# Optimization experiments

Hardware: AMD Instinct MI355X
Metric: run time of the kernel (lower is better)

## Reference

```python
import jax, jax.numpy as jnp
import numpy as np

B, N, NV = 2, 4096, 32768
HID = 128
XD, YD, ZD = 128, 128, 16  # dense occupancy grid dims (original derives from coord maxima)


def setup_inputs() -> dict:
    key = jax.random.key(0)
    ks = jax.random.split(key, 12)
    position = jax.random.normal(ks[0], (B, N, 3), jnp.float32) * 20.0
    scale = jax.random.uniform(ks[1], (B, N, 3), jnp.float32)
    rotation = jax.random.normal(ks[2], (B, N, 4), jnp.float32)
    opacity = jax.random.uniform(ks[3], (B, N, 1), jnp.float32)
    # sparse voxel coords: [batch_idx, x, y, z]
    b_idx = jax.random.randint(ks[4], (NV, 1), 0, B)
    xs = jax.random.randint(ks[5], (NV, 1), 0, XD)
    ys = jax.random.randint(ks[6], (NV, 1), 0, YD)
    zs = jax.random.randint(ks[7], (NV, 1), 0, ZD)
    voxel_coords = jnp.concatenate([b_idx, xs, ys, zs], axis=1).astype(jnp.int32)
    # MLP params: Linear(11,128) -> ReLU -> Linear(128,128)
    W1 = jax.random.normal(ks[8], (11, HID), jnp.float32) * (1.0 / np.sqrt(11))
    b1 = jnp.zeros((HID,), jnp.float32)
    W2 = jax.random.normal(ks[9], (HID, HID), jnp.float32) * (1.0 / np.sqrt(HID))
    b2 = jnp.zeros((HID,), jnp.float32)
    return {"position": position, "scale": scale, "rotation": rotation,
            "opacity": opacity, "W1": W1, "b1": b1, "W2": W2, "b2": b2,
            "voxel_coords": voxel_coords}


def reference(position, scale, rotation, opacity, W1, b1, W2, b2, voxel_coords):
    # concat gaussian attributes -> (B, N, 11)
    x = jnp.concatenate([position, scale, rotation, opacity], axis=-1)
    x = jnp.maximum(x @ W1 + b1, 0.0) @ W2 + b2  # (B, N, HID)

    # anchor grid: linspace(-50,50, N^(1/3))^3 -> (N, 3)
    n_side = int(round(N ** (1.0 / 3.0)))
    anchor_pos = jnp.linspace(-50.0, 50.0, n_side)
    grid = jnp.stack(jnp.meshgrid(anchor_pos, anchor_pos, anchor_pos, indexing="ij"), axis=-1)
    anchor_grid = grid.reshape(-1, 3)  # (N, 3)

    batch_ids = voxel_coords[:, 0]
    xyz = voxel_coords[:, 1:].astype(jnp.float32)  # (NV, 3)

    # Euclidean cdist (NV, N) via ||a||^2 + ||b||^2 - 2ab
    d2 = (jnp.sum(xyz * xyz, axis=1, keepdims=True)
          + jnp.sum(anchor_grid * anchor_grid, axis=1)[None, :]
          - 2.0 * (xyz @ anchor_grid.T))
    dist = jnp.sqrt(jnp.maximum(d2, 0.0))
    weight = jax.nn.softmax(-dist, axis=-1)  # (NV, N)

    fused = jnp.einsum("vn,bnd->bvd", weight, x)  # (B, NV, HID)

    # scatter into dense 5D occupancy grid (vectorized over all batches)
    occ = jnp.zeros((B, HID, XD, YD, ZD), jnp.float32)
    vals = fused[batch_ids, jnp.arange(NV)]  # (NV, HID) per-voxel feature from its own batch
    occ = occ.at[batch_ids, :, voxel_coords[:, 1], voxel_coords[:, 2], voxel_coords[:, 3]].set(vals)
    return occ
```

## Files before the change

kernel.cpp:

```cpp
#include <hip/hip_runtime.h>
#include <hip/hip_bf16.h>

#define B_    2
#define N_    4096
#define NV_   32768
#define HID_  128
#define XD_   128
#define YD_   128
#define ZD_   16
#define PLANE (XD_*YD_*ZD_)
#define LOCS  (B_*PLANE)
#define STEP  (100.0f/15.0f)
#define KS    4
#define VBL   160
#define L2E   1.4426950408889634f

typedef __attribute__((ext_vector_type(8)))  short short8;
typedef __attribute__((ext_vector_type(16))) float f32x16;

__device__ __forceinline__ float anchor_s(int i) {
    return fmaf((float)i, STEP * L2E, -50.0f * L2E);
}
__device__ __forceinline__ float fexp2(float x) {
    float r; asm("v_exp_f32 %0, %1" : "=v"(r) : "v"(x)); return r;
}
__device__ __forceinline__ unsigned short f2bf(float x) {
    unsigned u = __float_as_uint(x);
    return (unsigned short)((u + 0x7fffu + ((u >> 16) & 1u)) >> 16);
}
__device__ __forceinline__ void gload16(const void* g, void* l) {
    __builtin_amdgcn_global_load_lds(
        (const __attribute__((address_space(1))) unsigned int*)g,
        (__attribute__((address_space(3))) unsigned int*)l, 16, 0, 0);
}

__global__ __launch_bounds__(256) void mlp_kernel(
    const float* __restrict__ pos, const float* __restrict__ scl,
    const float* __restrict__ rot, const float* __restrict__ opa,
    const float* __restrict__ W1,  const float* __restrict__ b1,
    const float* __restrict__ W2,  const float* __restrict__ b2,
    unsigned short* __restrict__ xwT)
{
    int rg = threadIdx.x >> 7;
    int j  = threadIdx.x & 127;
    int r  = blockIdx.x * 2 + rg;
    __shared__ float sin_[2][11];
    __shared__ float h[2][HID_];
    if (j < 11) {
        float val;
        if (j < 3)       val = pos[r*3 + j];
        else if (j < 6)  val = scl[r*3 + (j-3)];
        else if (j < 10) val = rot[r*4 + (j-6)];
        else             val = opa[r];
        sin_[rg][j] = val;
    }
    __syncthreads();
    float a = b1[j];
    #pragma unroll
    for (int i = 0; i < 11; ++i) a = fmaf(sin_[rg][i], W1[i*HID_ + j], a);
    h[rg][j] = fmaxf(a, 0.0f);
    __syncthreads();
    float o = b2[j];
    for (int k = 0; k < HID_; ++k) o = fmaf(h[rg][k], W2[k*HID_ + j], o);
    int b = r >> 12, n = r & 4095;
    xwT[((size_t)(b*HID_ + j))*N_ + n] = f2bf(o);
}

__global__ __launch_bounds__(256) void scatter_kernel(
    const int* __restrict__ vc, int* __restrict__ map,
    int* __restrict__ cnt, int* __restrict__ vlist)
{
    int v = blockIdx.x * 256 + threadIdx.x;
    int4 c = ((const int4*)vc)[v];
    int loc = ((c.x*XD_ + c.y)*YD_ + c.z)*ZD_ + c.w;
    atomicMax(&map[loc], v);
    int lane = threadIdx.x & 63;
    unsigned long long m1 = __ballot(c.x != 0);
    unsigned long long mymask = c.x ? m1 : ~m1;
    int leader = (int)__ffsll(mymask) - 1;
    int total  = __popcll(mymask);
    int rank   = __popcll(mymask & ((1ull << lane) - 1ull));
    int base = 0;
    if (lane == leader) base = atomicAdd(&cnt[c.x], total);
    base = __shfl(base, leader);
    vlist[c.x*NV_ + base + rank] = v;
}

__global__ __launch_bounds__(256) void ml_kernel(
    const int* __restrict__ vc, float2* __restrict__ ml)
{
    int gid = blockIdx.x * 256 + threadIdx.x;
    int v = gid >> 3, sub = gid & 7;
    int4 c = ((const int4*)vc)[v];
    float vx = (float)c.y * L2E, vy = (float)c.z * L2E, vz = (float)c.w * L2E;
    float dz2_[16];
    #pragma unroll 16
    for (int iz = 0; iz < 16; ++iz) { float t = vz - anchor_s(iz); dz2_[iz] = t*t; }

    float m = 1e30f, l = 0.0f;
    #pragma unroll
    for (int i = 0; i < 2; ++i) {
        float dx = vx - anchor_s(sub*2 + i);
        float dx2 = dx*dx;
        for (int iy = 0; iy < 16; ++iy) {
            float dy = vy - anchor_s(iy);
            float bxy = fmaf(dy, dy, dx2);
            #pragma unroll 16
            for (int iz = 0; iz < 16; ++iz) {
                float d = sqrtf(bxy + dz2_[iz]);
                float dm = d - m;
                float e = fexp2(-fabsf(dm));
                bool nm = dm < 0.0f;
                l = nm ? fmaf(l, e, 1.0f) : (l + e);
                m = nm ? d : m;
            }
        }
    }
    #pragma unroll
    for (int off = 1; off < 8; off <<= 1) {
        float m2 = __shfl_xor(m, off);
        float l2 = __shfl_xor(l, off);
        float mn = fminf(m, m2);
        l = l * fexp2(mn - m) + l2 * fexp2(mn - m2);
        m = mn;
    }
    if (sub == 0) ml[v] = make_float2(m, 1.0f / l);
}

__global__ __launch_bounds__(256) void fuse_kernel(
    const unsigned short* __restrict__ xwT, const float2* __restrict__ ml,
    const int* __restrict__ vc,   const int* __restrict__ vlist,
    const int* __restrict__ cnt,  float* __restrict__ fused_p)
{
    int bid  = blockIdx.x;
    int ks_  = bid & (KS-1);
    int rest = bid >> 2;
    int seg  = (rest >= VBL) ? 1 : 0;
    int bi   = rest - seg*VBL;
    int count = cnt[seg];
    int vbase = bi * 128;
    if (vbase >= count) return;
    int nv = min(128, count - vbase);
    int k0 = ks_ * (N_/KS);

    __shared__ __align__(16) unsigned char sXT[16384];
    __shared__ int svid[128];

    int tid = threadIdx.x;
    int w  = tid >> 6, l = tid & 63;
    int h  = l >> 5;
    int cl = l & 31;

    if (tid < 128) svid[tid] = (tid < nv) ? vlist[seg*NV_ + vbase + tid] : -1;

    int vloc = w*32 + cl;
    float pml = -1e30f, pvx = 0.f, pvy = 0.f;
    float dz2_[16];
    #pragma unroll 16
    for (int iz = 0; iz < 16; ++iz) dz2_[iz] = 0.f;
    if (vloc < nv) {
        int vid = vlist[seg*NV_ + vbase + vloc];
        int4 c = ((const int4*)vc)[vid];
        pvx = (float)c.y * L2E; pvy = (float)c.z * L2E;
        float pvz = (float)c.w * L2E;
        pml = ml[vid].x;
        #pragma unroll 16
        for (int iz = 0; iz < 16; ++iz) { float t = pvz - anchor_s(iz); dz2_[iz] = t*t; }
    }

    int d0s  = w*32 + (l >> 3);
    int blkX = (l & 7) ^ ((l >> 3) & 7);
    const unsigned short* sb = xwT + (size_t)(seg*128 + d0s)*N_ + blkX*8 + k0;
    char* ldsb = (char*)sXT + (size_t)(w*4)*1024;

    f32x16 acc[4];
    #pragma unroll
    for (int i = 0; i < 4; ++i) acc[i] = (f32x16)(0.f);

    for (int t = 0; t < (N_/KS)/64; ++t) {
        __syncthreads();
        #pragma unroll
        for (int i = 0; i < 4; ++i)
            gload16(sb + (size_t)i*8*N_ + t*64, ldsb + i*1024);

        unsigned pk_[4][4];
        int nb = k0 + t*64;
        #pragma unroll
        for (int kss = 0; kss < 4; ++kss) {
            int kg = nb + kss*16;
            float ax = anchor_s(kg >> 8);
            float ay = anchor_s((kg >> 4) & 15);
            float dx = pvx - ax, dy = pvy - ay;
            float bxy = fmaf(dx, dx, dy*dy);
            #pragma unroll
            for (int jj = 0; jj < 4; ++jj) {
                float dA = sqrtf(bxy + dz2_[h*8 + 2*jj]);
                float dB = sqrtf(bxy + dz2_[h*8 + 2*jj + 1]);
                float p0 = fexp2(pml - dA);
                float p1 = fexp2(pml - dB);
                asm("v_cvt_pk_bf16_f32 %0, %1, %2" : "=v"(pk_[kss][jj]) : "v"(p0), "v"(p1));
            }
        }
        __syncthreads();

        #pragma unroll
        for (int kss = 0; kss < 4; ++kss) {
            union { uint4 q; short8 s; } u8;
            u8.q = make_uint4(pk_[kss][0], pk_[kss][1], pk_[kss][2], pk_[kss][3]);
            short8 af = u8.s;
            #pragma unroll
            for (int df = 0; df < 4; ++df) {
                int row = df*32 + cl;
                int blk = (kss*2 + h) ^ (row & 7);
                short8 bf = *(const short8*)&sXT[row*128 + blk*16];
                acc[df] = __builtin_amdgcn_mfma_f32_32x32x16_bf16(af, bf, acc[df], 0, 0, 0);
            }
        }
    }

    float* fp = fused_p + (size_t)ks_ * NV_ * HID_;
    #pragma unroll
    for (int df = 0; df < 4; ++df) {
        int dcol = df*32 + cl;
        #pragma unroll
        for (int reg = 0; reg < 16; ++reg) {
            int vrow = w*32 + (reg & 3) + 8*(reg >> 2) + 4*h;
            int sv = svid[vrow];
            if (sv >= 0) fp[(size_t)sv*HID_ + dcol] = acc[df][reg];
        }
    }
}

__global__ __launch_bounds__(256) void out_kernel(
    const int* __restrict__ map, const float* __restrict__ fused_p,
    const float2* __restrict__ ml, float* __restrict__ out)
{
    int q = blockIdx.x * 256 + threadIdx.x;
    int loc0 = q << 2;
    int b   = loc0 >> 18;
    int rem = loc0 & (PLANE - 1);
    int4 vv = ((const int4*)map)[q];
    size_t obase = ((size_t)b * HID_) * PLANE + rem;
    const size_t S4 = (size_t)NV_ * HID_ / 4;
    const float4* P = (const float4*)fused_p;

    int   va[4] = {vv.x, vv.y, vv.z, vv.w};
    float il[4];
    const float4* rp[4];
    #pragma unroll
    for (int k = 0; k < 4; ++k) {
        il[k] = (va[k] >= 0) ? ml[va[k]].y : 0.0f;
        rp[k] = P + (size_t)(va[k] >= 0 ? va[k] : 0) * 32;
    }

    for (int chb = 0; chb < 32; ++chb) {
        float4 vals[4];
        #pragma unroll
        for (int k = 0; k < 4; ++k) {
            float4 s = make_float4(0.f, 0.f, 0.f, 0.f);
            if (va[k] >= 0) {
                float4 a = rp[k][chb];
                float4 bq = rp[k][chb + S4];
                float4 cq = rp[k][chb + 2*S4];
                float4 dq = rp[k][chb + 3*S4];
                s.x = (a.x + bq.x + cq.x + dq.x) * il[k];
                s.y = (a.y + bq.y + cq.y + dq.y) * il[k];
                s.z = (a.z + bq.z + cq.z + dq.z) * il[k];
                s.w = (a.w + bq.w + cq.w + dq.w) * il[k];
            }
            vals[k] = s;
        }
        *(float4*)&out[obase + (size_t)(chb*4 + 0) * PLANE] = make_float4(vals[0].x, vals[1].x, vals[2].x, vals[3].x);
        *(float4*)&out[obase + (size_t)(chb*4 + 1) * PLANE] = make_float4(vals[0].y, vals[1].y, vals[2].y, vals[3].y);
        *(float4*)&out[obase + (size_t)(chb*4 + 2) * PLANE] = make_float4(vals[0].z, vals[1].z, vals[2].z, vals[3].z);
        *(float4*)&out[obase + (size_t)(chb*4 + 3) * PLANE] = make_float4(vals[0].w, vals[1].w, vals[2].w, vals[3].w);
    }
}

extern "C" void kernel_launch(void* const* d_in, const int* in_sizes, int n_in,
                              void* d_out, int out_size, void* d_ws, size_t ws_size,
                              hipStream_t stream) {
    const float* pos = (const float*)d_in[0];
    const float* scl = (const float*)d_in[1];
    const float* rot = (const float*)d_in[2];
    const float* opa = (const float*)d_in[3];
    const float* W1  = (const float*)d_in[4];
    const float* b1  = (const float*)d_in[5];
    const float* W2  = (const float*)d_in[6];
    const float* b2  = (const float*)d_in[7];
    const int*   vc  = (const int*)d_in[8];
    float* out = (float*)d_out;

    char* ws = (char*)d_ws;
    unsigned short* xwT = (unsigned short*)(ws);
    float2* ml      = (float2*)(ws + (2u<<20));
    float*  fused_p = (float*) (ws + (4u<<20));
    int*    map     = (int*)   (ws + (72u<<20));
    int*    vlist   = (int*)   (ws + (74u<<20));
    int*    cnt     = (int*)   (ws + (75u<<20));

    hipMemsetAsync(map, 0xFF, LOCS*sizeof(int), stream);
    hipMemsetAsync(cnt, 0, 2*sizeof(int), stream);

    mlp_kernel<<<(B_*N_)/2, 256, 0, stream>>>(pos, scl, rot, opa, W1, b1, W2, b2, xwT);
    scatter_kernel<<<NV_/256, 256, 0, stream>>>(vc, map, cnt, vlist);
    ml_kernel<<<(NV_*8)/256, 256, 0, stream>>>(vc, ml);
    fuse_kernel<<<2*VBL*KS, 256, 0, stream>>>(xwT, ml, vc, vlist, cnt, fused_p);
    out_kernel<<<LOCS/(256*4), 256, 0, stream>>>(map, fused_p, ml, out);
}
```

Measured before the change: 312.0 us.

## Batch MLP rows, fuse scatter into ml, double-buffer fuse, add split-K reduce kernel

The MLP kernel now handles 8 rows per block and reuses each W2 load across 4 rows. The scatter kernel is folded into the ml kernel. The ml kernel now does a two-pass softmax normaliser: an exact min distance first, then summing only the anchor rows within a cutoff. The fuse kernel double-buffers the LDS tile loads so the next tile loads while MFMA runs, and uses nontemporal stores. A separate reduce kernel collapses the split-K partials so the dense out_kernel reads a single compact row. The distance cutoff slightly approximates the normaliser, and the extra kernel adds one more round trip through memory.

Result: no change. 317.2 us (+1.6%).

```diff
diff --git a/kernel.cpp b/kernel.cpp
--- a/kernel.cpp
+++ b/kernel.cpp
@@ -17,6 +17,7 @@
 
 typedef __attribute__((ext_vector_type(8)))  short short8;
 typedef __attribute__((ext_vector_type(16))) float f32x16;
+typedef __attribute__((ext_vector_type(4)))  float fv4;
 
 __device__ __forceinline__ float anchor_s(int i) {
     return fmaf((float)i, STEP * L2E, -50.0f * L2E);
@@ -41,89 +42,124 @@
     const float* __restrict__ W2,  const float* __restrict__ b2,
     unsigned short* __restrict__ xwT)
 {
-    int rg = threadIdx.x >> 7;
-    int j  = threadIdx.x & 127;
-    int r  = blockIdx.x * 2 + rg;
-    __shared__ float sin_[2][11];
-    __shared__ float h[2][HID_];
-    if (j < 11) {
+    int tid = threadIdx.x;
+    int j  = tid & 127;
+    int rg = tid >> 7;
+    int r0 = blockIdx.x * 8;
+    __shared__ float sin_[8][11];
+    __shared__ float h[8][HID_];
+    if (tid < 88) {
+        int rr = tid / 11, c = tid - rr*11;
+        int r = r0 + rr;
         float val;
-        if (j < 3)       val = pos[r*3 + j];
-        else if (j < 6)  val = scl[r*3 + (j-3)];
-        else if (j < 10) val = rot[r*4 + (j-6)];
+        if (c < 3)       val = pos[r*3 + c];
+        else if (c < 6)  val = scl[r*3 + (c-3)];
+        else if (c < 10) val = rot[r*4 + (c-6)];
         else             val = opa[r];
-        sin_[rg][j] = val;
+        sin_[rr][c] = val;
     }
     __syncthreads();
-    float a = b1[j];
-    #pragma unroll
-    for (int i = 0; i < 11; ++i) a = fmaf(sin_[rg][i], W1[i*HID_ + j], a);
-    h[rg][j] = fmaxf(a, 0.0f);
+    float bb1 = b1[j];
+    #pragma unroll
+    for (int q = 0; q < 4; ++q) {
+        int rr = rg*4 + q;
+        float a = bb1;
+        #pragma unroll
+        for (int i = 0; i < 11; ++i) a = fmaf(sin_[rr][i], W1[i*HID_ + j], a);
+        h[rr][j] = fmaxf(a, 0.0f);
+    }
     __syncthreads();
-    float o = b2[j];
-    for (int k = 0; k < HID_; ++k) o = fmaf(h[rg][k], W2[k*HID_ + j], o);
-    int b = r >> 12, n = r & 4095;
-    xwT[((size_t)(b*HID_ + j))*N_ + n] = f2bf(o);
-}
-
-__global__ __launch_bounds__(256) void scatter_kernel(
-    const int* __restrict__ vc, int* __restrict__ map,
-    int* __restrict__ cnt, int* __restrict__ vlist)
-{
-    int v = blockIdx.x * 256 + threadIdx.x;
-    int4 c = ((const int4*)vc)[v];
-    int loc = ((c.x*XD_ + c.y)*YD_ + c.z)*ZD_ + c.w;
-    atomicMax(&map[loc], v);
-    int lane = threadIdx.x & 63;
-    unsigned long long m1 = __ballot(c.x != 0);
-    unsigned long long mymask = c.x ? m1 : ~m1;
-    int leader = (int)__ffsll(mymask) - 1;
-    int total  = __popcll(mymask);
-    int rank   = __popcll(mymask & ((1ull << lane) - 1ull));
-    int base = 0;
-    if (lane == leader) base = atomicAdd(&cnt[c.x], total);
-    base = __shfl(base, leader);
-    vlist[c.x*NV_ + base + rank] = v;
+    float bb2 = b2[j];
+    float o0 = bb2, o1 = bb2, o2 = bb2, o3 = bb2;
+    #pragma unroll 4
+    for (int k = 0; k < HID_; ++k) {
+        float w2 = W2[k*HID_ + j];
+        int rb = rg*4;
+        o0 = fmaf(h[rb+0][k], w2, o0);
+        o1 = fmaf(h[rb+1][k], w2, o1);
+        o2 = fmaf(h[rb+2][k], w2, o2);
+        o3 = fmaf(h[rb+3][k], w2, o3);
+    }
+    float o[4] = {o0, o1, o2, o3};
+    #pragma unroll
+    for (int q = 0; q < 4; ++q) {
+        int r = r0 + rg*4 + q;
+        int b = r >> 12, n = r & 4095;
+        xwT[((size_t)(b*HID_ + j))*N_ + n] = f2bf(o[q]);
+    }
 }
 
 __global__ __launch_bounds__(256) void ml_kernel(
-    const int* __restrict__ vc, float2* __restrict__ ml)
+    const int* __restrict__ vc, float2* __restrict__ ml,
+    int* __restrict__ map, int* __restrict__ cnt, int* __restrict__ vlist)
 {
     int gid = blockIdx.x * 256 + threadIdx.x;
     int v = gid >> 3, sub = gid & 7;
     int4 c = ((const int4*)vc)[v];
+
+    if (sub == 0) {
+        int loc = ((c.x*XD_ + c.y)*YD_ + c.z)*ZD_ + c.w;
+        atomicMax(&map[loc], v);
+        int lane = threadIdx.x & 63;
+        unsigned long long act = __ballot(1);
+        unsigned long long m1 = __ballot(c.x != 0);
+        unsigned long long mymask = c.x ? m1 : (act & ~m1);
+        int leader = (int)__ffsll(mymask) - 1;
+        int total  = __popcll(mymask);
+        int rank   = __popcll(mymask & ((1ull << lane) - 1ull));
+        int base = 0;
+        if (lane == leader) base = atomicAdd(&cnt[c.x], total);
+        base = __shfl(base, leader);
+        vlist[c.x*NV_ + base + rank] = v;
+    }
+
     float vx = (float)c.y * L2E, vy = (float)c.z * L2E, vz = (float)c.w * L2E;
     float dz2_[16];
+    float mindz2 = 1e30f;
     #pragma unroll 16
-    for (int iz = 0; iz < 16; ++iz) { float t = vz - anchor_s(iz); dz2_[iz] = t*t; }
-
-    float m = 1e30f, l = 0.0f;
+    for (int iz = 0; iz < 16; ++iz) {
+        float t = vz - anchor_s(iz); dz2_[iz] = t*t;
+        mindz2 = fminf(mindz2, dz2_[iz]);
+    }
+    float dxa = vx - anchor_s(sub*2), dxb = vx - anchor_s(sub*2 + 1);
+    float dx2_[2] = {dxa*dxa, dxb*dxb};
+
+    float md[4] = {1e30f, 1e30f, 1e30f, 1e30f};
     #pragma unroll
     for (int i = 0; i < 2; ++i) {
-        float dx = vx - anchor_s(sub*2 + i);
-        float dx2 = dx*dx;
         for (int iy = 0; iy < 16; ++iy) {
             float dy = vy - anchor_s(iy);
-            float bxy = fmaf(dy, dy, dx2);
+            float bxy = fmaf(dy, dy, dx2_[i]);
             #pragma unroll 16
-            for (int iz = 0; iz < 16; ++iz) {
-                float d = sqrtf(bxy + dz2_[iz]);
-                float dm = d - m;
-                float e = fexp2(-fabsf(dm));
-                bool nm = dm < 0.0f;
-                l = nm ? fmaf(l, e, 1.0f) : (l + e);
-                m = nm ? d : m;
+            for (int iz = 0; iz < 16; ++iz)
+                md[iz & 3] = fminf(md[iz & 3], bxy + dz2_[iz]);
+        }
+    }
+    float m2v = fminf(fminf(md[0], md[1]), fminf(md[2], md[3]));
+    #pragma unroll
+    for (int off = 1; off < 8; off <<= 1) m2v = fminf(m2v, __shfl_xor(m2v, off));
+    float m = sqrtf(m2v);
+
+    float lim = m + 34.0f;
+    float lim2 = lim * lim;
+    float la = 0.f, lb = 0.f;
+    #pragma unroll
+    for (int i = 0; i < 2; ++i) {
+        for (int iy = 0; iy < 16; ++iy) {
+            float dy = vy - anchor_s(iy);
+            float bxy = fmaf(dy, dy, dx2_[i]);
+            if (bxy + mindz2 <= lim2) {
+                #pragma unroll 8
+                for (int iz = 0; iz < 16; iz += 2) {
+                    la += fexp2(m - sqrtf(bxy + dz2_[iz]));
+                    lb += fexp2(m - sqrtf(bxy + dz2_[iz+1]));
+                }
             }
         }
     }
-    #pragma unroll
-    for (int off = 1; off < 8; off <<= 1) {
-        float m2 = __shfl_xor(m, off);
-        float l2 = __shfl_xor(l, off);
-        float mn = fminf(m, m2);
-        l = l * fexp2(mn - m) + l2 * fexp2(mn - m2);
-        m = mn;
-    }
+    float l = la + lb;
+    #pragma unroll
+    for (int off = 1; off < 8; off <<= 1) l += __shfl_xor(l, off);
     if (sub == 0) ml[v] = make_float2(m, 1.0f / l);
 }
 
@@ -143,7 +179,7 @@
     int nv = min(128, count - vbase);
     int k0 = ks_ * (N_/KS);
 
-    __shared__ __align__(16) unsigned char sXT[16384];
+    __shared__ __align__(16) unsigned char sXT[2][16384];
     __shared__ int svid[128];
 
     int tid = threadIdx.x;
@@ -171,18 +207,23 @@
     int d0s  = w*32 + (l >> 3);
     int blkX = (l & 7) ^ ((l >> 3) & 7);
     const unsigned short* sb = xwT + (size_t)(seg*128 + d0s)*N_ + blkX*8 + k0;
-    char* ldsb = (char*)sXT + (size_t)(w*4)*1024;
-
-    f32x16 acc[4];
-    #pragma unroll
-    for (int i = 0; i < 4; ++i) acc[i] = (f32x16)(0.f);
-
-    for (int t = 0; t < (N_/KS)/64; ++t) {
-        __syncthreads();
+
+    auto stage = [&](int bsel, int t) {
+        char* ldsb = (char*)&sXT[bsel][0] + w*4096;
         #pragma unroll
         for (int i = 0; i < 4; ++i)
             gload16(sb + (size_t)i*8*N_ + t*64, ldsb + i*1024);
-
+    };
+
+    f32x16 acc[4];
+    #pragma unroll
+    for (int i = 0; i < 4; ++i) acc[i] = (f32x16)(0.f);
+
+    const int TILES = (N_/KS)/64;
+    stage(0, 0);
+
+    for (int t = 0; t < TILES; ++t) {
+        int cur = t & 1;
         unsigned pk_[4][4];
         int nb = k0 + t*64;
         #pragma unroll
@@ -202,7 +243,7 @@
             }
         }
         __syncthreads();
-
+        if (t + 1 < TILES) stage(cur ^ 1, t + 1);
         #pragma unroll
         for (int kss = 0; kss < 4; ++kss) {
             union { uint4 q; short8 s; } u8;
@@ -212,7 +253,7 @@
             for (int df = 0; df < 4; ++df) {
                 int row = df*32 + cl;
                 int blk = (kss*2 + h) ^ (row & 7);
-                short8 bf = *(const short8*)&sXT[row*128 + blk*16];
+                short8 bf = *(const short8*)&sXT[cur][row*128 + blk*16];
                 acc[df] = __builtin_amdgcn_mfma_f32_32x32x16_bf16(af, bf, acc[df], 0, 0, 0);
             }
         }
@@ -226,54 +267,58 @@
         for (int reg = 0; reg < 16; ++reg) {
             int vrow = w*32 + (reg & 3) + 8*(reg >> 2) + 4*h;
             int sv = svid[vrow];
-            if (sv >= 0) fp[(size_t)sv*HID_ + dcol] = acc[df][reg];
-        }
-    }
+            if (sv >= 0)
+                __builtin_nontemporal_store(acc[df][reg], &fp[(size_t)sv*HID_ + dcol]);
+        }
+    }
+}
+
+__global__ __launch_bounds__(256) void reduce_kernel(
+    const float* __restrict__ fused_p, const float2* __restrict__ ml,
+    float* __restrict__ fused)
+{
+    int idx = blockIdx.x * 256 + threadIdx.x;
+    int v = idx >> 5;
+    float il = ml[v].y;
+    const size_t stride = (size_t)NV_ * HID_ / 4;
+    const fv4* p = (const fv4*)fused_p + idx;
+    fv4 a = __builtin_nontemporal_load(&p[0]);
+    fv4 b = __builtin_nontemporal_load(&p[stride]);
+    fv4 c = __builtin_nontemporal_load(&p[2*stride]);
+    fv4 d = __builtin_nontemporal_load(&p[3*stride]);
+    fv4 o = (a + b + c + d) * il;
+    ((fv4*)fused)[idx] = o;
 }
 
 __global__ __launch_bounds__(256) void out_kernel(
-    const int* __restrict__ map, const float* __restrict__ fused_p,
-    const float2* __restrict__ ml, float* __restrict__ out)
+    const int* __restrict__ map, const float* __restrict__ fused,
+    float* __restrict__ out)
 {
     int q = blockIdx.x * 256 + threadIdx.x;
     int loc0 = q << 2;
     int b   = loc0 >> 18;
     int rem = loc0 & (PLANE - 1);
     int4 vv = ((const int4*)map)[q];
+    const fv4* r0 = (const fv4*)(fused + (size_t)(vv.x < 0 ? 0 : vv.x) * HID_);
+    const fv4* r1 = (const fv4*)(fused + (size_t)(vv.y < 0 ? 0 : vv.y) * HID_);
+    const fv4* r2 = (const fv4*)(fused + (size_t)(vv.z < 0 ? 0 : vv.z) * HID_);
+    const fv4* r3 = (const fv4*)(fused + (size_t)(vv.w < 0 ? 0 : vv.w) * HID_);
     size_t obase = ((size_t)b * HID_) * PLANE + rem;
-    const size_t S4 = (size_t)NV_ * HID_ / 4;
-    const float4* P = (const float4*)fused_p;
-
-    int   va[4] = {vv.x, vv.y, vv.z, vv.w};
-    float il[4];
-    const float4* rp[4];
-    #pragma unroll
-    for (int k = 0; k < 4; ++k) {
-        il[k] = (va[k] >= 0) ? ml[va[k]].y : 0.0f;
-        rp[k] = P + (size_t)(va[k] >= 0 ? va[k] : 0) * 32;
-    }
-
+    const fv4 z4 = (fv4)(0.f);
+    #pragma unroll 4
     for (int chb = 0; chb < 32; ++chb) {
-        float4 vals[4];
-        #pragma unroll
-        for (int k = 0; k < 4; ++k) {
-            float4 s = make_float4(0.f, 0.f, 0.f, 0.f);
-            if (va[k] >= 0) {
-                float4 a = rp[k][chb];
-                float4 bq = rp[k][chb + S4];
-                float4 cq = rp[k][chb + 2*S4];
-                float4 dq = rp[k][chb + 3*S4];
-                s.x = (a.x + bq.x + cq.x + dq.x) * il[k];
-                s.y = (a.y + bq.y + cq.y + dq.y) * il[k];
-                s.z = (a.z + bq.z + cq.z + dq.z) * il[k];
-                s.w = (a.w + bq.w + cq.w + dq.w) * il[k];
-            }
-            vals[k] = s;
-        }
-        *(float4*)&out[obase + (size_t)(chb*4 + 0) * PLANE] = make_float4(vals[0].x, vals[1].x, vals[2].x, vals[3].x);
-        *(float4*)&out[obase + (size_t)(chb*4 + 1) * PLANE] = make_float4(vals[0].y, vals[1].y, vals[2].y, vals[3].y);
-        *(float4*)&out[obase + (size_t)(chb*4 + 2) * PLANE] = make_float4(vals[0].z, vals[1].z, vals[2].z, vals[3].z);
-        *(float4*)&out[obase + (size_t)(chb*4 + 3) * PLANE] = make_float4(vals[0].w, vals[1].w, vals[2].w, vals[3].w);
+        fv4 a = (vv.x >= 0) ? r0[chb] : z4;
+        fv4 c = (vv.y >= 0) ? r1[chb] : z4;
+        fv4 d = (vv.z >= 0) ? r2[chb] : z4;
+        fv4 e = (vv.w >= 0) ? r3[chb] : z4;
+        fv4 o0 = {a.x, c.x, d.x, e.x};
+        fv4 o1 = {a.y, c.y, d.y, e.y};
+        fv4 o2 = {a.z, c.z, d.z, e.z};
+        fv4 o3 = {a.w, c.w, d.w, e.w};
+        __builtin_nontemporal_store(o0, (fv4*)&out[obase + (size_t)(chb*4 + 0) * PLANE]);
+        __builtin_nontemporal_store(o1, (fv4*)&out[obase + (size_t)(chb*4 + 1) * PLANE]);
+        __builtin_nontemporal_store(o2, (fv4*)&out[obase + (size_t)(chb*4 + 2) * PLANE]);
+        __builtin_nontemporal_store(o3, (fv4*)&out[obase + (size_t)(chb*4 + 3) * PLANE]);
     }
 }
 
@@ -294,17 +339,18 @@
     char* ws = (char*)d_ws;
     unsigned short* xwT = (unsigned short*)(ws);
     float2* ml      = (float2*)(ws + (2u<<20));
-    float*  fused_p = (float*) (ws + (4u<<20));
-    int*    map     = (int*)   (ws + (72u<<20));
-    int*    vlist   = (int*)   (ws + (74u<<20));
-    int*    cnt     = (int*)   (ws + (75u<<20));
+    float*  fused   = (float*) (ws + (4u<<20));
+    float*  fused_p = (float*) (ws + (20u<<20));
+    int*    map     = (int*)   (ws + (84u<<20));
+    int*    vlist   = (int*)   (ws + (86u<<20));
+    int*    cnt     = (int*)   (ws + (87u<<20));
 
     hipMemsetAsync(map, 0xFF, LOCS*sizeof(int), stream);
     hipMemsetAsync(cnt, 0, 2*sizeof(int), stream);
 
-    mlp_kernel<<<(B_*N_)/2, 256, 0, stream>>>(pos, scl, rot, opa, W1, b1, W2, b2, xwT);
-    scatter_kernel<<<NV_/256, 256, 0, stream>>>(vc, map, cnt, vlist);
-    ml_kernel<<<(NV_*8)/256, 256, 0, stream>>>(vc, ml);
+    mlp_kernel<<<(B_*N_)/8, 256, 0, stream>>>(pos, scl, rot, opa, W1, b1, W2, b2, xwT);
+    ml_kernel<<<(NV_*8)/256, 256, 0, stream>>>(vc, ml, map, cnt, vlist);
     fuse_kernel<<<2*VBL*KS, 256, 0, stream>>>(xwT, ml, vc, vlist, cnt, fused_p);
-    out_kernel<<<LOCS/(256*4), 256, 0, stream>>>(map, fused_p, ml, out);
-}
+    reduce_kernel<<<(NV_*HID_/4)/256, 256, 0, stream>>>(fused_p, ml, fused);
+    out_kernel<<<LOCS/(256*4), 256, 0, stream>>>(map, fused, out);
+}
```
